# Optimization experiments

Hardware: AMD Instinct MI355X
Metric: run time of the kernel (lower is better)

The kernel has to match this reference:

```python
import jax, jax.numpy as jnp
import numpy as np

NEG = -999999.0

def setup_inputs() -> dict:
    key = jax.random.key(0)
    ks = jax.random.split(key, 8)
    B, N, H, D = 8, 2048, 1, 256  # in_dim = H*D = 256
    in_dim = H * D
    feat_in = jax.random.normal(ks[0], (B, N, in_dim), dtype=jnp.float32)
    adj = jax.random.randint(ks[1], (B, N, N), 0, 2, dtype=jnp.int32)
    # parameters (xavier-ish scales)
    W  = jax.random.normal(ks[2], (H, in_dim, D), dtype=jnp.float32) * (2.0 / (in_dim + D)) ** 0.5
    b  = jnp.zeros((D,), dtype=jnp.float32)
    Ws = jax.random.normal(ks[3], (1, 2 * D), dtype=jnp.float32) * (2.0 / (2 * D + 1)) ** 0.5  # strengh.weight
    bs = jnp.zeros((1,), dtype=jnp.float32)                                                     # strengh.bias
    Hw = jax.random.normal(ks[4], (in_dim, in_dim), dtype=jnp.float32) * (1.0 / in_dim) ** 0.5  # H.weight
    Hb = jnp.zeros((in_dim,), dtype=jnp.float32)                                                # H.bias
    return {"feat_in": feat_in, "adj": adj, "W": W, "b": b, "Ws": Ws, "bs": bs, "Hw": Hw, "Hb": Hb}

def reference(feat_in, adj, W, b, Ws, bs, Hw, Hb):
    B, N, in_dim = feat_in.shape
    H, _, D = W.shape
    h = jnp.einsum('bni,hid->bhnd', feat_in, W)                    # [B,H,N,D]
    # strengh(cat(h_src, h_dst)) decomposed: H_src[b,i,j]=h[b,i], H_dst[b,i,j]=h[b,j]
    ws_src, ws_dst = Ws[0, :D], Ws[0, D:]
    a_src = jnp.einsum('bhnd,d->bhn', h, ws_src)                   # per row i
    a_dst = jnp.einsum('bhnd,d->bhn', h, ws_dst)                   # per col j
    attn = jax.nn.sigmoid(a_src[:, :, :, None] + a_dst[:, :, None, :] + bs[0])  # [B,H,N,N]
    strict_low = jnp.tril(jnp.ones((N, N), dtype=feat_in.dtype), -1)
    attn = attn * strict_low                                        # zero outside strict lower triangle
    I_A = jnp.eye(N, dtype=feat_in.dtype) - attn                    # [B,H,N,N]
    I_A_raw = I_A
    # allowed positions: lower triangle (incl diag) AND adj==1
    low = jnp.tril(jnp.ones((N, N), dtype=jnp.bool_), 0)
    allowed = low[None, None] & (adj[:, None] == 1)                 # [B,H,N,N]
    scores = jnp.where(allowed, I_A, NEG)
    P = jax.nn.softmax(scores, axis=-1)
    feat_out = jnp.einsum('bhij,bhjd->bhid', P, h) + b              # [B,H,N,D]
    feat_out = feat_out.transpose(0, 2, 1, 3).reshape(B, N, H * D)
    feat_out = jax.nn.elu(feat_out)
    gate = jax.nn.sigmoid(feat_in @ Hw.T + Hb)
    out = gate * feat_out + (1.0 - gate) * feat_in                  # dropout = identity (eval)
    return out, I_A_raw
```

## Files before the change

kernel.cpp:

```cpp
#include <hip/hip_runtime.h>
#include <math.h>

constexpr int Bc = 8, Nc = 2048, Dc = 256;
constexpr int BN = Bc * Nc;

typedef __attribute__((ext_vector_type(8))) short short8;
typedef __attribute__((ext_vector_type(4))) float f32x4;

__device__ __forceinline__ float sigmoidf_(float x) { return 1.0f / (1.0f + expf(-x)); }

__device__ __forceinline__ unsigned short f2bf(float f) {
    unsigned int u = __float_as_uint(f);
    u = (u + 0x7FFFu + ((u >> 16) & 1u)) >> 16;
    return (unsigned short)u;
}
__device__ __forceinline__ float bf2f(unsigned short s) {
    return __uint_as_float(((unsigned int)s) << 16);
}

__device__ __forceinline__ short8 ld_frag(const unsigned short* base) {
    ushort4 lo = *(const ushort4*)(base);
    ushort4 hi = *(const ushort4*)(base + 16);
    short8 a;
    a[0] = (short)lo.x; a[1] = (short)lo.y; a[2] = (short)lo.z; a[3] = (short)lo.w;
    a[4] = (short)hi.x; a[5] = (short)hi.y; a[6] = (short)hi.z; a[7] = (short)hi.w;
    return a;
}
__device__ __forceinline__ f32x4 fz4() { f32x4 z = {0.f, 0.f, 0.f, 0.f}; return z; }

__device__ __forceinline__ void lds_barrier() {
    asm volatile("s_waitcnt lgkmcnt(0)" ::: "memory");
    __builtin_amdgcn_s_barrier();
    __builtin_amdgcn_sched_barrier(0);
}

__global__ __launch_bounds__(256) void cast_kernel(const float* __restrict__ f,
                                                   unsigned short* __restrict__ o) {
    int i = (blockIdx.x * 256 + threadIdx.x) * 4;
    float4 v = *(const float4*)(f + i);
    ushort4 u = {f2bf(v.x), f2bf(v.y), f2bf(v.z), f2bf(v.w)};
    *(ushort4*)(o + i) = u;
}

__global__ __launch_bounds__(256) void pack_bt_kernel(const float* __restrict__ W,
                                                      const float* __restrict__ Hw,
                                                      unsigned short* __restrict__ BmT) {
    int idx = blockIdx.x * 256 + threadIdx.x;
    int o = idx >> 8, k = idx & 255;
    float v = (o < 256) ? W[k * 256 + o] : Hw[(o - 256) * 256 + k];
    BmT[idx] = f2bf(v);
}

__global__ __launch_bounds__(256) void gemm_lds(const unsigned short* __restrict__ featb,
                                                const unsigned short* __restrict__ BmT,
                                                const float* __restrict__ Hb,
                                                float* __restrict__ h,
                                                float* __restrict__ gate) {
    __shared__ unsigned short As[128][72];
    __shared__ unsigned short Bs[128][72];
    const int tid = threadIdx.x, lane = tid & 63, w = tid >> 6;
    const int g16 = lane >> 4, li = lane & 15;
    const int wr = w >> 1, wc = w & 1;
    const int m0 = blockIdx.x * 128, n0 = blockIdx.y * 128;
    const int srow = tid >> 1, sseg = (tid & 1) * 32;
    f32x4 acc[4][4];
#pragma unroll
    for (int rf = 0; rf < 4; ++rf)
#pragma unroll
        for (int cf = 0; cf < 4; ++cf) acc[rf][cf] = fz4();
    for (int k0 = 0; k0 < 256; k0 += 64) {
        if (k0) __syncthreads();
#pragma unroll
        for (int q = 0; q < 4; ++q) {
            int4 va = *(const int4*)(featb + (size_t)(m0 + srow) * 256 + k0 + sseg + q * 8);
            *(int4*)&As[srow][sseg + q * 8] = va;
            int4 vb = *(const int4*)(BmT + (size_t)(n0 + srow) * 256 + k0 + sseg + q * 8);
            *(int4*)&Bs[srow][sseg + q * 8] = vb;
        }
        __syncthreads();
#pragma unroll
        for (int ks = 0; ks < 2; ++ks) {
            short8 Af[4], Bf[4];
#pragma unroll
            for (int rf = 0; rf < 4; ++rf)
                Af[rf] = ld_frag(&As[wr * 64 + rf * 16 + li][ks * 32 + g16 * 4]);
#pragma unroll
            for (int cf = 0; cf < 4; ++cf)
                Bf[cf] = ld_frag(&Bs[wc * 64 + cf * 16 + li][ks * 32 + g16 * 4]);
#pragma unroll
            for (int rf = 0; rf < 4; ++rf)
#pragma unroll
                for (int cf = 0; cf < 4; ++cf)
                    acc[rf][cf] = __builtin_amdgcn_mfma_f32_16x16x32_bf16(Af[rf], Bf[cf], acc[rf][cf], 0, 0, 0);
        }
    }
#pragma unroll
    for (int rf = 0; rf < 4; ++rf)
#pragma unroll
        for (int cf = 0; cf < 4; ++cf) {
            const int n = n0 + wc * 64 + cf * 16 + li;
#pragma unroll
            for (int reg = 0; reg < 4; ++reg) {
                const int m = m0 + wr * 64 + rf * 16 + g16 * 4 + reg;
                float v = acc[rf][cf][reg];
                if (n < 256) h[(size_t)m * 256 + n] = v;
                else gate[(size_t)m * 256 + (n - 256)] = sigmoidf_(v + Hb[n - 256]);
            }
        }
}

__global__ __launch_bounds__(256) void tr64f_kernel(const float* __restrict__ h,
                                                    const float* __restrict__ Ws,
                                                    unsigned short* __restrict__ hT,
                                                    float* __restrict__ a_src,
                                                    float* __restrict__ a_dst,
                                                    float* __restrict__ mean_h) {
    __shared__ float tile[64][65];
    const int j0 = blockIdx.x * 64, d0 = blockIdx.y * 64, b = blockIdx.z;
    const int tid = threadIdx.x;
#pragma unroll
    for (int p = 0; p < 16; ++p) {
        int idx = tid + p * 256;
        int jl = idx >> 6, dl = idx & 63;
        tile[jl][dl] = h[((size_t)b * Nc + j0 + jl) * 256 + d0 + dl];
    }
    __syncthreads();
#pragma unroll
    for (int p = 0; p < 16; ++p) {
        int idx = tid + p * 256;
        int dl = idx >> 6, jl = idx & 63;
        hT[((size_t)b * 256 + d0 + dl) * Nc + j0 + jl] = f2bf(tile[jl][dl]);
    }
    {
        const int jl = tid >> 2, q = tid & 3;
        float s1 = 0.f, s2 = 0.f;
#pragma unroll
        for (int e = 0; e < 16; ++e) {
            const float hv = tile[jl][q * 16 + e];
            s1 = fmaf(hv, Ws[d0 + q * 16 + e], s1);
            s2 = fmaf(hv, Ws[256 + d0 + q * 16 + e], s2);
        }
        s1 += __shfl_xor(s1, 1); s1 += __shfl_xor(s1, 2);
        s2 += __shfl_xor(s2, 1); s2 += __shfl_xor(s2, 2);
        if (q == 0) {
            atomicAdd(&a_src[b * Nc + j0 + jl], s1);
            atomicAdd(&a_dst[b * Nc + j0 + jl], s2);
        }
    }
    {
        const int dl = tid & 63, part = tid >> 6;
        float sm = 0.f;
#pragma unroll
        for (int e = 0; e < 16; ++e) sm += tile[part * 16 + e][dl];
        atomicAdd(&mean_h[b * 256 + d0 + dl], sm);
    }
}

__global__ __launch_bounds__(256) void fill_kernel(float* __restrict__ out2) {
    const int b = blockIdx.x & 7, ib = blockIdx.x >> 3;
    const int j0 = (ib + 1) * 32;
    if (j0 >= Nc) return;
    const int i0 = ib * 32;
    const int w4 = (Nc - j0) >> 2;
    const float4 z = make_float4(0.f, 0.f, 0.f, 0.f);
    for (int r = 0; r < 32; ++r) {
        float4* row = (float4*)(out2 + ((size_t)b * Nc + i0 + r) * Nc + j0);
        for (int jc = threadIdx.x; jc < w4; jc += 256) row[jc] = z;
    }
}

constexpr int CHUNK = 8;
__global__ __launch_bounds__(256) void score64(
    const int* __restrict__ adj, const unsigned short* __restrict__ hT,
    const float* __restrict__ a_src, const float* __restrict__ a_dst,
    const float* __restrict__ bs_p, float* __restrict__ out2,
    float* __restrict__ accO, float* __restrict__ sArr) {
    __shared__ unsigned short pt[32][72];
    __shared__ float sh_as[32];

    const int bid = blockIdx.x;
    const int b = bid & 7;
    int t = bid >> 3;
    int g = 0;
    while (g < 7 && 4 * (g + 1) * (g + 2) <= t) ++g;
    const int r_ = t - 4 * g * (g + 1);
    const int ib = g * 8 + r_ / (g + 1);
    const int c = r_ % (g + 1);
    const int i0 = ib * 32;
    const int t0 = c * CHUNK;
    const int t1 = min(ib + 1, t0 + CHUNK);

    const int tid = threadIdx.x, lane = tid & 63, w = tid >> 6;
    const int g16 = lane >> 4, li = lane & 15;
    const int jj = tid & 31, r0 = tid >> 5;
    const float bsv = bs_p[0];

    if (tid < 32) sh_as[tid] = a_src[b * Nc + i0 + tid];
    __syncthreads();
    float asv[4];
#pragma unroll
    for (int q = 0; q < 4; ++q) asv[q] = sh_as[r0 + 8 * q];

    const int* adjb = adj + (size_t)b * Nc * Nc;
    const float* adb = a_dst + b * Nc;
    const unsigned short* hTb = hT + (size_t)b * 256 * Nc;

    f32x4 acc[2][4];
#pragma unroll
    for (int rf = 0; rf < 2; ++rf)
#pragma unroll
        for (int cf = 0; cf < 4; ++cf) acc[rf][cf] = fz4();
    f32x4 sacc0 = fz4(), sacc1 = fz4();
    short8 ones;
#pragma unroll
    for (int e = 0; e < 8; ++e) ones[e] = (short)0x3F80;

    int pre_aj[2][4];
    float pre_ad[2];
#define PREF(TT, NS)                                                                   \
    {                                                                                  \
        _Pragma("unroll") for (int s = 0; s < 2; ++s) if (s < (NS)) {                  \
            pre_ad[s] = adb[((TT) + s) * 32 + jj];                                     \
            _Pragma("unroll") for (int q = 0; q < 4; ++q)                              \
                pre_aj[s][q] = adjb[(size_t)(i0 + r0 + 8 * q) * Nc + ((TT) + s) * 32 + jj]; \
        }                                                                              \
    }

    PREF(t0, min(2, t1 - t0));
    for (int tt = t0; tt < t1; tt += 2) {
        const int ns = min(2, t1 - tt);
        int aj_[2][4];
        float ad_[2];
#pragma unroll
        for (int s = 0; s < 2; ++s) {
            ad_[s] = pre_ad[s];
#pragma unroll
            for (int q = 0; q < 4; ++q) aj_[s][q] = pre_aj[s][q];
        }
        if (tt + 2 < t1) PREF(tt + 2, min(2, t1 - tt - 2));
        short8 Bf[2][4];
#pragma unroll
        for (int s = 0; s < 2; ++s)
            if (s < ns) {
#pragma unroll
                for (int cf = 0; cf < 4; ++cf)
                    Bf[s][cf] = ld_frag(hTb + (size_t)(w * 64 + cf * 16 + li) * Nc + (tt + s) * 32 + g16 * 4);
            }
#pragma unroll
        for (int s = 0; s < 2; ++s)
            if (s < ns) {
                const int jt = tt + s;
                const int j = jt * 32 + jj;
                const bool dia = (jt == ib);
#pragma unroll
                for (int q = 0; q < 4; ++q) {
                    const int r = r0 + 8 * q;
                    const int irow = i0 + r;
                    const float IA = -__builtin_amdgcn_rcpf(1.f + __expf(-(asv[q] + ad_[s] + bsv)));
                    float o2v, p;
                    if (dia && j > irow) { o2v = 0.f; p = 0.f; }
                    else if (dia && j == irow) { o2v = 1.f; p = (aj_[s][q] == 1) ? 1.f : 0.f; }
                    else { o2v = IA; p = (aj_[s][q] == 1) ? __expf(IA - 1.f) : 0.f; }
                    out2[((size_t)b * Nc + irow) * Nc + j] = o2v;
                    pt[r][s * 32 + jj] = f2bf(p);
                }
            }
        lds_barrier();
#pragma unroll
        for (int s = 0; s < 2; ++s)
            if (s < ns) {
                short8 A0 = ld_frag(&pt[li][s * 32 + g16 * 4]);
                short8 A1 = ld_frag(&pt[16 + li][s * 32 + g16 * 4]);
                if (w == 0) {
                    sacc0 = __builtin_amdgcn_mfma_f32_16x16x32_bf16(A0, ones, sacc0, 0, 0, 0);
                    sacc1 = __builtin_amdgcn_mfma_f32_16x16x32_bf16(A1, ones, sacc1, 0, 0, 0);
                }
#pragma unroll
                for (int cf = 0; cf < 4; ++cf) {
                    acc[0][cf] = __builtin_amdgcn_mfma_f32_16x16x32_bf16(A0, Bf[s][cf], acc[0][cf], 0, 0, 0);
                    acc[1][cf] = __builtin_amdgcn_mfma_f32_16x16x32_bf16(A1, Bf[s][cf], acc[1][cf], 0, 0, 0);
                }
            }
        lds_barrier();
    }
#undef PREF
#pragma unroll
    for (int rf = 0; rf < 2; ++rf)
#pragma unroll
        for (int cf = 0; cf < 4; ++cf) {
            float* dst = accO + ((size_t)b * Nc + i0 + rf * 16 + g16 * 4) * 256 + w * 64 + cf * 16 + li;
#pragma unroll
            for (int reg = 0; reg < 4; ++reg)
                atomicAdd(dst + (size_t)reg * 256, acc[rf][cf][reg]);
        }
    if (w == 0 && li == 0) {
#pragma unroll
        for (int reg = 0; reg < 4; ++reg) {
            atomicAdd(&sArr[b * Nc + i0 + g16 * 4 + reg], sacc0[reg]);
            atomicAdd(&sArr[b * Nc + i0 + 16 + g16 * 4 + reg], sacc1[reg]);
        }
    }
}

__global__ __launch_bounds__(256) void epilogue_kernel(
    const float* __restrict__ gate, const float* __restrict__ feat,
    const float* __restrict__ bvec, const float* __restrict__ mean_h,
    const float* __restrict__ sArr, float* __restrict__ out1) {
    const int row = blockIdx.x * 4 + (threadIdx.x >> 6);
    const int lane = threadIdx.x & 63;
    const int b = row >> 11;
    const size_t g = (size_t)row * 256;
    const float s = sArr[row];
    float4 v;
    if (s == 0.f) {
        float4 mh = ((const float4*)(mean_h + b * 256))[lane];
        const float inv = 1.0f / Nc;
        v.x = mh.x * inv; v.y = mh.y * inv; v.z = mh.z * inv; v.w = mh.w * inv;
    } else {
        float4 a = ((const float4*)(out1 + g))[lane];
        const float inv = 1.0f / s;
        v.x = a.x * inv; v.y = a.y * inv; v.z = a.z * inv; v.w = a.w * inv;
    }
    const float4 b4 = ((const float4*)bvec)[lane];
    v.x += b4.x; v.y += b4.y; v.z += b4.z; v.w += b4.w;
    v.x = v.x > 0.f ? v.x : __expf(v.x) - 1.f;
    v.y = v.y > 0.f ? v.y : __expf(v.y) - 1.f;
    v.z = v.z > 0.f ? v.z : __expf(v.z) - 1.f;
    v.w = v.w > 0.f ? v.w : __expf(v.w) - 1.f;
    const float4 g4 = ((const float4*)(gate + g))[lane];
    const float4 f4 = ((const float4*)(feat + g))[lane];
    float4 o;
    o.x = g4.x * v.x + (1.f - g4.x) * f4.x;
    o.y = g4.y * v.y + (1.f - g4.y) * f4.y;
    o.z = g4.z * v.z + (1.f - g4.z) * f4.z;
    o.w = g4.w * v.w + (1.f - g4.w) * f4.w;
    ((float4*)(out1 + g))[lane] = o;
}

extern "C" void kernel_launch(void* const* d_in, const int* in_sizes, int n_in,
                              void* d_out, int out_size, void* d_ws, size_t ws_size,
                              hipStream_t stream) {
    const float* feat = (const float*)d_in[0];
    const int* adj = (const int*)d_in[1];
    const float* W = (const float*)d_in[2];
    const float* bvec = (const float*)d_in[3];
    const float* Ws = (const float*)d_in[4];
    const float* bs = (const float*)d_in[5];
    const float* Hw = (const float*)d_in[6];
    const float* Hb = (const float*)d_in[7];

    float* ws = (float*)d_ws;
    unsigned short* featb = (unsigned short*)ws;
    unsigned short* hT = featb;
    unsigned short* BmT = featb + 4194304;
    float* h = ws + 2097152 + 65536;
    float* gate = h + 4194304;
    float* a_src = gate + 4194304;
    float* a_dst = a_src + 16384;
    float* mean_h = a_dst + 16384;
    float* sArr = mean_h + 2048;

    float* out1 = (float*)d_out;
    float* out2 = out1 + (size_t)BN * 256;

    hipLaunchKernelGGL(cast_kernel, dim3(4096), dim3(256), 0, stream, feat, featb);
    hipLaunchKernelGGL(pack_bt_kernel, dim3(512), dim3(256), 0, stream, W, Hw, BmT);
    hipLaunchKernelGGL(gemm_lds, dim3(128, 4), dim3(256), 0, stream, featb, BmT, Hb, h, gate);
    hipMemsetAsync(a_src, 0, (16384 + 16384 + 2048 + 16384) * sizeof(float), stream);
    hipLaunchKernelGGL(tr64f_kernel, dim3(32, 4, 8), dim3(256), 0, stream,
                       h, Ws, hT, a_src, a_dst, mean_h);
    hipMemsetAsync(out1, 0, (size_t)BN * 256 * sizeof(float), stream);
    hipLaunchKernelGGL(fill_kernel, dim3(512), dim3(256), 0, stream, out2);
    hipLaunchKernelGGL(score64, dim3(2304), dim3(256), 0, stream,
                       adj, hT, a_src, a_dst, bs, out2, out1, sArr);
    hipLaunchKernelGGL(epilogue_kernel, dim3(4096), dim3(256), 0, stream,
                       gate, feat, bvec, mean_h, sArr, out1);
}
```

Measured before the change: 389.3 us.

## Fuse bf16 cast into GEMM, zero-fill into score kernel, double-buffer P tile

Removes the separate cast kernel: the GEMM now loads fp32 features and converts them to bf16 while staging into LDS. The separate upper-triangle zero-fill kernel is folded into score64, with each block zeroing a slice of its row band. score64 now uses a larger chunk size with balanced splitting across blocks, giving 1280 blocks instead of 2304. It also double-buffers the P tile in LDS so one barrier per iteration can be dropped. These cut launch count and redundant traffic, but each GEMM block now reads twice the feature bytes and work per block is less even.

```diff
diff --git a/kernel.cpp b/kernel.cpp
--- a/kernel.cpp
+++ b/kernel.cpp
@@ -34,14 +34,6 @@
     __builtin_amdgcn_sched_barrier(0);
 }
 
-__global__ __launch_bounds__(256) void cast_kernel(const float* __restrict__ f,
-                                                   unsigned short* __restrict__ o) {
-    int i = (blockIdx.x * 256 + threadIdx.x) * 4;
-    float4 v = *(const float4*)(f + i);
-    ushort4 u = {f2bf(v.x), f2bf(v.y), f2bf(v.z), f2bf(v.w)};
-    *(ushort4*)(o + i) = u;
-}
-
 __global__ __launch_bounds__(256) void pack_bt_kernel(const float* __restrict__ W,
                                                       const float* __restrict__ Hw,
                                                       unsigned short* __restrict__ BmT) {
@@ -51,7 +43,7 @@
     BmT[idx] = f2bf(v);
 }
 
-__global__ __launch_bounds__(256) void gemm_lds(const unsigned short* __restrict__ featb,
+__global__ __launch_bounds__(256) void gemm_lds(const float* __restrict__ featf,
                                                 const unsigned short* __restrict__ BmT,
                                                 const float* __restrict__ Hb,
                                                 float* __restrict__ h,
@@ -62,7 +54,7 @@
     const int g16 = lane >> 4, li = lane & 15;
     const int wr = w >> 1, wc = w & 1;
     const int m0 = blockIdx.x * 128, n0 = blockIdx.y * 128;
-    const int srow = tid >> 1, sseg = (tid & 1) * 32;
+    const int srow = tid >> 1, fseg = (tid & 1) * 32;
     f32x4 acc[4][4];
 #pragma unroll
     for (int rf = 0; rf < 4; ++rf)
@@ -71,11 +63,15 @@
     for (int k0 = 0; k0 < 256; k0 += 64) {
         if (k0) __syncthreads();
 #pragma unroll
+        for (int q = 0; q < 8; ++q) {
+            float4 va = *(const float4*)(featf + (size_t)(m0 + srow) * 256 + k0 + fseg + q * 4);
+            ushort4 u = {f2bf(va.x), f2bf(va.y), f2bf(va.z), f2bf(va.w)};
+            *(ushort4*)&As[srow][fseg + q * 4] = u;
+        }
+#pragma unroll
         for (int q = 0; q < 4; ++q) {
-            int4 va = *(const int4*)(featb + (size_t)(m0 + srow) * 256 + k0 + sseg + q * 8);
-            *(int4*)&As[srow][sseg + q * 8] = va;
-            int4 vb = *(const int4*)(BmT + (size_t)(n0 + srow) * 256 + k0 + sseg + q * 8);
-            *(int4*)&Bs[srow][sseg + q * 8] = vb;
+            int4 vb = *(const int4*)(BmT + (size_t)(n0 + srow) * 256 + k0 + fseg + q * 8);
+            *(int4*)&Bs[srow][fseg + q * 8] = vb;
         }
         __syncthreads();
 #pragma unroll
@@ -156,50 +152,36 @@
     }
 }
 
-__global__ __launch_bounds__(256) void fill_kernel(float* __restrict__ out2) {
-    const int b = blockIdx.x & 7, ib = blockIdx.x >> 3;
-    const int j0 = (ib + 1) * 32;
-    if (j0 >= Nc) return;
-    const int i0 = ib * 32;
-    const int w4 = (Nc - j0) >> 2;
-    const float4 z = make_float4(0.f, 0.f, 0.f, 0.f);
-    for (int r = 0; r < 32; ++r) {
-        float4* row = (float4*)(out2 + ((size_t)b * Nc + i0 + r) * Nc + j0);
-        for (int jc = threadIdx.x; jc < w4; jc += 256) row[jc] = z;
-    }
-}
-
-constexpr int CHUNK = 8;
+constexpr int CHUNK = 16;
 __global__ __launch_bounds__(256) void score64(
     const int* __restrict__ adj, const unsigned short* __restrict__ hT,
     const float* __restrict__ a_src, const float* __restrict__ a_dst,
     const float* __restrict__ bs_p, float* __restrict__ out2,
     float* __restrict__ accO, float* __restrict__ sArr) {
-    __shared__ unsigned short pt[32][72];
-    __shared__ float sh_as[32];
+    __shared__ unsigned short pt[2][32][72];
 
     const int bid = blockIdx.x;
     const int b = bid & 7;
     int t = bid >> 3;
     int g = 0;
-    while (g < 7 && 4 * (g + 1) * (g + 2) <= t) ++g;
-    const int r_ = t - 4 * g * (g + 1);
-    const int ib = g * 8 + r_ / (g + 1);
+    while (g < 3 && 8 * (g + 1) * (g + 2) <= t) ++g;
+    const int r_ = t - 8 * g * (g + 1);
+    const int ib = g * 16 + r_ / (g + 1);
     const int c = r_ % (g + 1);
+    const int nch = g + 1;
     const int i0 = ib * 32;
-    const int t0 = c * CHUNK;
-    const int t1 = min(ib + 1, t0 + CHUNK);
+    const int T = ib + 1;
+    const int base = T / nch, rem = T % nch;
+    const int t0 = c * base + min(c, rem);
+    const int t1 = t0 + base + (c < rem ? 1 : 0);
 
     const int tid = threadIdx.x, lane = tid & 63, w = tid >> 6;
     const int g16 = lane >> 4, li = lane & 15;
     const int jj = tid & 31, r0 = tid >> 5;
     const float bsv = bs_p[0];
-
-    if (tid < 32) sh_as[tid] = a_src[b * Nc + i0 + tid];
-    __syncthreads();
     float asv[4];
 #pragma unroll
-    for (int q = 0; q < 4; ++q) asv[q] = sh_as[r0 + 8 * q];
+    for (int q = 0; q < 4; ++q) asv[q] = a_src[b * Nc + i0 + r0 + 8 * q];
 
     const int* adjb = adj + (size_t)b * Nc * Nc;
     const float* adb = a_dst + b * Nc;
@@ -227,7 +209,8 @@
     }
 
     PREF(t0, min(2, t1 - t0));
-    for (int tt = t0; tt < t1; tt += 2) {
+    int p = 0;
+    for (int tt = t0; tt < t1; tt += 2, p ^= 1) {
         const int ns = min(2, t1 - tt);
         int aj_[2][4];
         float ad_[2];
@@ -257,20 +240,20 @@
                     const int r = r0 + 8 * q;
                     const int irow = i0 + r;
                     const float IA = -__builtin_amdgcn_rcpf(1.f + __expf(-(asv[q] + ad_[s] + bsv)));
-                    float o2v, p;
-                    if (dia && j > irow) { o2v = 0.f; p = 0.f; }
-                    else if (dia && j == irow) { o2v = 1.f; p = (aj_[s][q] == 1) ? 1.f : 0.f; }
-                    else { o2v = IA; p = (aj_[s][q] == 1) ? __expf(IA - 1.f) : 0.f; }
+                    float o2v, pp;
+                    if (dia && j > irow) { o2v = 0.f; pp = 0.f; }
+                    else if (dia && j == irow) { o2v = 1.f; pp = (aj_[s][q] == 1) ? 1.f : 0.f; }
+                    else { o2v = IA; pp = (aj_[s][q] == 1) ? __expf(IA - 1.f) : 0.f; }
                     out2[((size_t)b * Nc + irow) * Nc + j] = o2v;
-                    pt[r][s * 32 + jj] = f2bf(p);
+                    pt[p][r][s * 32 + jj] = f2bf(pp);
                 }
             }
         lds_barrier();
 #pragma unroll
         for (int s = 0; s < 2; ++s)
             if (s < ns) {
-                short8 A0 = ld_frag(&pt[li][s * 32 + g16 * 4]);
-                short8 A1 = ld_frag(&pt[16 + li][s * 32 + g16 * 4]);
+                short8 A0 = ld_frag(&pt[p][li][s * 32 + g16 * 4]);
+                short8 A1 = ld_frag(&pt[p][16 + li][s * 32 + g16 * 4]);
                 if (w == 0) {
                     sacc0 = __builtin_amdgcn_mfma_f32_16x16x32_bf16(A0, ones, sacc0, 0, 0, 0);
                     sacc1 = __builtin_amdgcn_mfma_f32_16x16x32_bf16(A1, ones, sacc1, 0, 0, 0);
@@ -281,7 +264,6 @@
                     acc[1][cf] = __builtin_amdgcn_mfma_f32_16x16x32_bf16(A1, Bf[s][cf], acc[1][cf], 0, 0, 0);
                 }
             }
-        lds_barrier();
     }
 #undef PREF
 #pragma unroll
@@ -298,6 +280,17 @@
         for (int reg = 0; reg < 4; ++reg) {
             atomicAdd(&sArr[b * Nc + i0 + g16 * 4 + reg], sacc0[reg]);
             atomicAdd(&sArr[b * Nc + i0 + 16 + g16 * 4 + reg], sacc1[reg]);
+        }
+    }
+    {
+        const int w4beg = (i0 + 32) >> 2;
+        const int W4 = 512 - w4beg;
+        const int sbeg = w4beg + (int)(((long)W4 * c) / nch);
+        const int send = w4beg + (int)(((long)W4 * (c + 1)) / nch);
+        const float4 z = make_float4(0.f, 0.f, 0.f, 0.f);
+        for (int r = 0; r < 32; ++r) {
+            float4* rowp = (float4*)(out2 + ((size_t)b * Nc + i0 + r) * Nc);
+            for (int j4 = sbeg + tid; j4 < send; j4 += 256) rowp[j4] = z;
         }
     }
 }
@@ -350,9 +343,8 @@
     const float* Hb = (const float*)d_in[7];
 
     float* ws = (float*)d_ws;
-    unsigned short* featb = (unsigned short*)ws;
-    unsigned short* hT = featb;
-    unsigned short* BmT = featb + 4194304;
+    unsigned short* hT = (unsigned short*)ws;
+    unsigned short* BmT = hT + 4194304;
     float* h = ws + 2097152 + 65536;
     float* gate = h + 4194304;
     float* a_src = gate + 4194304;
@@ -363,15 +355,13 @@
     float* out1 = (float*)d_out;
     float* out2 = out1 + (size_t)BN * 256;
 
-    hipLaunchKernelGGL(cast_kernel, dim3(4096), dim3(256), 0, stream, feat, featb);
+    hipMemsetAsync(a_src, 0, (16384 + 16384 + 2048 + 16384) * sizeof(float), stream);
     hipLaunchKernelGGL(pack_bt_kernel, dim3(512), dim3(256), 0, stream, W, Hw, BmT);
-    hipLaunchKernelGGL(gemm_lds, dim3(128, 4), dim3(256), 0, stream, featb, BmT, Hb, h, gate);
-    hipMemsetAsync(a_src, 0, (16384 + 16384 + 2048 + 16384) * sizeof(float), stream);
+    hipLaunchKernelGGL(gemm_lds, dim3(128, 4), dim3(256), 0, stream, feat, BmT, Hb, h, gate);
     hipLaunchKernelGGL(tr64f_kernel, dim3(32, 4, 8), dim3(256), 0, stream,
                        h, Ws, hT, a_src, a_dst, mean_h);
     hipMemsetAsync(out1, 0, (size_t)BN * 256 * sizeof(float), stream);
-    hipLaunchKernelGGL(fill_kernel, dim3(512), dim3(256), 0, stream, out2);
-    hipLaunchKernelGGL(score64, dim3(2304), dim3(256), 0, stream,
+    hipLaunchKernelGGL(score64, dim3(1280), dim3(256), 0, stream,
                        adj, hT, a_src, a_dst, bs, out2, out1, sArr);
     hipLaunchKernelGGL(epilogue_kernel, dim3(4096), dim3(256), 0, stream,
                        gate, feat, bvec, mean_h, sArr, out1);
```

After: 388.0 us. About the same (-0.4%).
